# Kernel optimization log

Measured on AMD Instinct MI355X. Metric: run time of the kernel, lower is better.

## Reference

```python
import jax, jax.numpy as jnp
import numpy as np
from jax import lax

B, L, D, F = 32, 512, 256, 256
K = 3
EPS = 1e-5


def _layer_norm(h, g, b):
    mu = jnp.mean(h, axis=-1, keepdims=True)
    var = jnp.var(h, axis=-1, keepdims=True)
    return (h - mu) * lax.rsqrt(var + EPS) * g + b


def _conv1d(h, w, b):
    # h: [B, L, Cin], w: [K, Cin, Cout] -> [B, L, Cout], 'same' padding (pad=1, k=3)
    return lax.conv_general_dilated(h, w, window_strides=(1,), padding=[(1, 1)],
                                    dimension_numbers=('NWC', 'WIO', 'NWC')) + b


def _duration_predictor(x, c1w, c1b, ln1g, ln1b, c2w, c2b, ln2g, ln2b, lw, lb):
    h = jax.nn.relu(_layer_norm(_conv1d(x, c1w, c1b), ln1g, ln1b))
    h = jax.nn.relu(_layer_norm(_conv1d(h, c2w, c2b), ln2g, ln2b))
    d = jax.nn.relu(h @ lw + lb)  # [B, L, 1]
    return d[..., 0]              # [B, L] (squeeze, training mode)


def _expand_one(xb, dur, M):
    # xb: [L, D], dur: [L] int. Repeat row i dur[i] times, zero-pad to M frames.
    cs = jnp.cumsum(dur)                              # [L]
    t = jnp.arange(M)                                 # [M]
    idx = jnp.searchsorted(cs, t, side='right')       # phoneme id per frame
    valid = t < cs[-1]
    out = jnp.take(xb, jnp.clip(idx, 0, xb.shape[0] - 1), axis=0)
    return jnp.where(valid[:, None], out, jnp.zeros((), xb.dtype))


def setup_inputs() -> dict:
    key = jax.random.key(0)
    ks = jax.random.split(key, 8)
    s_c = 1.0 / np.sqrt(K * F)
    s_l = 1.0 / np.sqrt(F)
    return {
        'x': jax.random.normal(ks[0], (B, L, D), jnp.float32),
        'durations': jax.random.randint(ks[1], (B, L), 0, 7),
        'mel_max_length': 4096,
        'conv1_w': jax.random.normal(ks[2], (K, D, F), jnp.float32) * s_c,
        'conv1_b': jnp.zeros((F,), jnp.float32),
        'ln1_g': jnp.ones((F,), jnp.float32),
        'ln1_b': jnp.zeros((F,), jnp.float32),
        'conv2_w': jax.random.normal(ks[3], (K, F, F), jnp.float32) * s_c,
        'conv2_b': jnp.zeros((F,), jnp.float32),
        'ln2_g': jnp.ones((F,), jnp.float32),
        'ln2_b': jnp.zeros((F,), jnp.float32),
        'lin_w': jax.random.normal(ks[4], (F, 1), jnp.float32) * s_l,
        'lin_b': jnp.zeros((1,), jnp.float32),
    }


def reference(x, durations, mel_max_length, conv1_w, conv1_b, ln1_g, ln1_b,
              conv2_w, conv2_b, ln2_g, ln2_b, lin_w, lin_b):
    dur_pred = _duration_predictor(x, conv1_w, conv1_b, ln1_g, ln1_b,
                                   conv2_w, conv2_b, ln2_g, ln2_b, lin_w, lin_b)
    dur = durations.astype(jnp.int32)
    output = jax.vmap(lambda xb, db: _expand_one(xb, db, mel_max_length))(x, dur)
    return output, dur_pred
```

## Files before the change

### kernel.cpp

```cpp
#include <hip/hip_runtime.h>

typedef __attribute__((ext_vector_type(8))) short short8;
typedef __attribute__((ext_vector_type(4))) float f32x4;

#define BATCH 32
#define LSEQ  512
#define DIN   256
#define FDIM  256
#define KTOT  768
#define MT    32
#define BK    32
#define PADA  264

__device__ __forceinline__ short f2bf(float f) {
    union { float f; unsigned u; } v; v.f = f;
    unsigned r = v.u + 0x7FFFu + ((v.u >> 16) & 1u);
    return (short)(r >> 16);
}

__global__ __launch_bounds__(512)
void prep_kernel(const int* __restrict__ dur, int* __restrict__ cs,
                 const float* __restrict__ w1, const float* __restrict__ w2,
                 short* __restrict__ wt1, short* __restrict__ wt2) {
    __shared__ int s[LSEQ];
    const int t = threadIdx.x, b = blockIdx.x;
    if (b < BATCH) {
        s[t] = dur[b * LSEQ + t];
        __syncthreads();
        for (int off = 1; off < LSEQ; off <<= 1) {
            int v = (t >= off) ? s[t - off] : 0;
            __syncthreads();
            s[t] += v;
            __syncthreads();
        }
        cs[b * LSEQ + t] = s[t];
    } else {
        const int id = (b - BATCH) * 512 + t;
        const int n = id & 255, k = id >> 8;
        const int dst = (((k >> 5) * FDIM) + n) * BK + (k & 31);
        wt1[dst] = f2bf(w1[id]);
        wt2[dst] = f2bf(w2[id]);
    }
}

template<bool AF32, bool FUSE>
__global__ __launch_bounds__(256)
void conv_ln(const void* __restrict__ Asrc, const short* __restrict__ Bt,
             const float* __restrict__ cb, const float* __restrict__ g,
             const float* __restrict__ bta, const float* __restrict__ lw,
             const float* __restrict__ lb, short* __restrict__ Hout,
             float* __restrict__ Dout)
{
    __shared__ short As[34][PADA];
    __shared__ float redS[MT][4];
    __shared__ float redQ[MT][4];
    __shared__ float redD[MT][4];
    __shared__ float muS[MT];
    __shared__ float rsS[MT];

    const int tid  = threadIdx.x;
    const int wave = tid >> 6;
    const int lane = tid & 63;
    const int ml   = lane & 15;
    const int q    = lane >> 4;
    const int row0 = blockIdx.x * MT;
    const int bb   = row0 >> 9;
    const int r0   = row0 & (LSEQ - 1);

    for (int idx = tid; idx < 34 * 32; idx += 256) {
        const int r = idx >> 5, part = idx & 31;
        const int l2 = r0 + r - 1;
        short8 v = {0, 0, 0, 0, 0, 0, 0, 0};
        if (l2 >= 0 && l2 < LSEQ) {
            const size_t off = ((size_t)(bb * LSEQ + l2)) * DIN + part * 8;
            if (AF32) {
                const float4* s4 = (const float4*)((const float*)Asrc + off);
                float4 u0 = s4[0], u1 = s4[1];
                v[0] = f2bf(u0.x); v[1] = f2bf(u0.y); v[2] = f2bf(u0.z); v[3] = f2bf(u0.w);
                v[4] = f2bf(u1.x); v[5] = f2bf(u1.y); v[6] = f2bf(u1.z); v[7] = f2bf(u1.w);
            } else {
                v = *(const short8*)((const short*)Asrc + off);
            }
        }
        *(short8*)&As[r][part * 8] = v;
    }
    __syncthreads();

    f32x4 acc[2][4];
    #pragma unroll
    for (int mt = 0; mt < 2; mt++)
        #pragma unroll
        for (int nt = 0; nt < 4; nt++)
            #pragma unroll
            for (int r = 0; r < 4; r++)
                acc[mt][nt][r] = 0.f;

    const short* bptr = Bt + (size_t)(wave * 64 + ml) * BK + q * 8;
    #pragma unroll 1
    for (int tap = 0; tap < 3; tap++) {
        #pragma unroll
        for (int cc = 0; cc < 8; cc++) {
            short8 af0 = *(const short8*)&As[ml + tap][cc * 32 + q * 8];
            short8 af1 = *(const short8*)&As[16 + ml + tap][cc * 32 + q * 8];
            short8 b0 = *(const short8*)(bptr + 0 * 16 * BK);
            short8 b1 = *(const short8*)(bptr + 1 * 16 * BK);
            short8 b2 = *(const short8*)(bptr + 2 * 16 * BK);
            short8 b3 = *(const short8*)(bptr + 3 * 16 * BK);
            bptr += FDIM * BK;
            acc[0][0] = __builtin_amdgcn_mfma_f32_16x16x32_bf16(af0, b0, acc[0][0], 0, 0, 0);
            acc[0][1] = __builtin_amdgcn_mfma_f32_16x16x32_bf16(af0, b1, acc[0][1], 0, 0, 0);
            acc[0][2] = __builtin_amdgcn_mfma_f32_16x16x32_bf16(af0, b2, acc[0][2], 0, 0, 0);
            acc[0][3] = __builtin_amdgcn_mfma_f32_16x16x32_bf16(af0, b3, acc[0][3], 0, 0, 0);
            acc[1][0] = __builtin_amdgcn_mfma_f32_16x16x32_bf16(af1, b0, acc[1][0], 0, 0, 0);
            acc[1][1] = __builtin_amdgcn_mfma_f32_16x16x32_bf16(af1, b1, acc[1][1], 0, 0, 0);
            acc[1][2] = __builtin_amdgcn_mfma_f32_16x16x32_bf16(af1, b2, acc[1][2], 0, 0, 0);
            acc[1][3] = __builtin_amdgcn_mfma_f32_16x16x32_bf16(af1, b3, acc[1][3], 0, 0, 0);
        }
    }

    float cbv[4], gv[4], bv[4], lwv[4];
    #pragma unroll
    for (int nt = 0; nt < 4; nt++) {
        const int col = wave * 64 + nt * 16 + ml;
        cbv[nt] = cb[col]; gv[nt] = g[col]; bv[nt] = bta[col];
        lwv[nt] = FUSE ? lw[col] : 0.f;
    }
    #pragma unroll
    for (int mt = 0; mt < 2; mt++)
        #pragma unroll
        for (int nt = 0; nt < 4; nt++)
            #pragma unroll
            for (int r = 0; r < 4; r++)
                acc[mt][nt][r] += cbv[nt];

    #pragma unroll
    for (int mt = 0; mt < 2; mt++)
        #pragma unroll
        for (int r = 0; r < 4; r++) {
            float ps = 0.f, pq = 0.f;
            #pragma unroll
            for (int nt = 0; nt < 4; nt++) { float v = acc[mt][nt][r]; ps += v; pq += v * v; }
            #pragma unroll
            for (int d = 1; d < 16; d <<= 1) { ps += __shfl_xor(ps, d); pq += __shfl_xor(pq, d); }
            if (ml == 0) { const int row = mt * 16 + q * 4 + r; redS[row][wave] = ps; redQ[row][wave] = pq; }
        }
    __syncthreads();
    if (tid < MT) {
        float S = 0.f, Q = 0.f;
        #pragma unroll
        for (int w = 0; w < 4; w++) { S += redS[tid][w]; Q += redQ[tid][w]; }
        const float mu  = S * (1.f / 256.f);
        const float var = Q * (1.f / 256.f) - mu * mu;
        muS[tid] = mu; rsS[tid] = rsqrtf(var + 1e-5f);
    }
    __syncthreads();

    if (!FUSE) {
        #pragma unroll
        for (int mt = 0; mt < 2; mt++)
            #pragma unroll
            for (int r = 0; r < 4; r++) {
                const int row = mt * 16 + q * 4 + r;
                const float mu = muS[row], rs = rsS[row];
                #pragma unroll
                for (int nt = 0; nt < 4; nt++) {
                    const int col = wave * 64 + nt * 16 + ml;
                    float v = (acc[mt][nt][r] - mu) * rs * gv[nt] + bv[nt];
                    v = fmaxf(v, 0.f);
                    Hout[(size_t)(row0 + row) * FDIM + col] = f2bf(v);
                }
            }
    } else {
        #pragma unroll
        for (int mt = 0; mt < 2; mt++)
            #pragma unroll
            for (int r = 0; r < 4; r++) {
                const int row = mt * 16 + q * 4 + r;
                const float mu = muS[row], rs = rsS[row];
                float pd = 0.f;
                #pragma unroll
                for (int nt = 0; nt < 4; nt++) {
                    float v = (acc[mt][nt][r] - mu) * rs * gv[nt] + bv[nt];
                    v = fmaxf(v, 0.f);
                    pd += v * lwv[nt];
                }
                #pragma unroll
                for (int d = 1; d < 16; d <<= 1) pd += __shfl_xor(pd, d);
                if (ml == 0) redD[row][wave] = pd;
            }
        __syncthreads();
        if (tid < MT) {
            float Dv = 0.f;
            #pragma unroll
            for (int w = 0; w < 4; w++) Dv += redD[tid][w];
            Dout[row0 + tid] = fmaxf(Dv + lb[0], 0.f);
        }
    }
}

__global__ __launch_bounds__(256)
void expand_kernel(const float4* __restrict__ x4, const int* __restrict__ cs,
                   float4* __restrict__ out4, int M) {
    const int fr   = blockIdx.x * 4 + (threadIdx.x >> 6);
    const int lane = threadIdx.x & 63;
    const int b = fr / M;
    const int t = fr - b * M;
    const int* csb = cs + b * LSEQ;
    const int total = csb[LSEQ - 1];
    const size_t obase = (size_t)fr * 64 + lane;
    if (t < total) {
        int lo = 0, hi = LSEQ;
        while (lo < hi) { const int mid = (lo + hi) >> 1; if (csb[mid] > t) hi = mid; else lo = mid + 1; }
        const int idx = lo < LSEQ ? lo : LSEQ - 1;
        out4[obase] = x4[((size_t)(b * LSEQ + idx)) * 64 + lane];
    } else {
        out4[obase] = make_float4(0.f, 0.f, 0.f, 0.f);
    }
}

extern "C" void kernel_launch(void* const* d_in, const int* in_sizes, int n_in,
                              void* d_out, int out_size, void* d_ws, size_t ws_size,
                              hipStream_t stream)
{
    const float* x   = (const float*)d_in[0];
    const int*   dur = (const int*)d_in[1];
    const float* c1w = (const float*)d_in[3];
    const float* c1b = (const float*)d_in[4];
    const float* g1  = (const float*)d_in[5];
    const float* b1  = (const float*)d_in[6];
    const float* c2w = (const float*)d_in[7];
    const float* c2b = (const float*)d_in[8];
    const float* g2  = (const float*)d_in[9];
    const float* b2  = (const float*)d_in[10];
    const float* lw  = (const float*)d_in[11];
    const float* lb  = (const float*)d_in[12];

    const int M = (out_size - BATCH * LSEQ) / (BATCH * DIN);
    float* out     = (float*)d_out;
    float* dur_out = out + (size_t)BATCH * M * DIN;

    char* ws   = (char*)d_ws;
    int*   cs  = (int*)ws;
    short* wt1 = (short*)(ws + (64 << 10));
    short* wt2 = (short*)(ws + (64 << 10) + (384 << 10));
    short* h1  = (short*)(ws + (64 << 10) + 2 * (384 << 10));

    hipLaunchKernelGGL(prep_kernel, dim3(BATCH + (KTOT * FDIM) / 512), dim3(512), 0, stream,
                       dur, cs, c1w, c2w, wt1, wt2);
    hipLaunchKernelGGL((conv_ln<true, false>), dim3((BATCH * LSEQ) / MT), dim3(256), 0, stream,
                       (const void*)x, wt1, c1b, g1, b1, (const float*)nullptr, (const float*)nullptr,
                       h1, (float*)nullptr);
    hipLaunchKernelGGL((conv_ln<false, true>), dim3((BATCH * LSEQ) / MT), dim3(256), 0, stream,
                       (const void*)h1, wt2, c2b, g2, b2, lw, lb,
                       (short*)nullptr, dur_out);
    hipLaunchKernelGGL(expand_kernel, dim3((BATCH * M) / 4), dim3(256), 0, stream,
                       (const float4*)x, cs, (float4*)d_out, M);
}
```

Baseline: 214.9 us.

## Precompute frame index map and split expand work into conv kernels

The prep kernel now scatters a per-frame source row index (or -1 for padding) instead of storing cumulative sums, so expansion becomes a direct gather with no binary search. The standalone expand kernel is removed, and its blocks are split between the two conv+layernorm kernels as extra leading blocks. The aim is to overlap memory-bound output writes with compute-bound conv work and drop one launch. In exchange, the prep kernel does serial per-phoneme writes and initialises M entries per batch, and the workspace grows.

```diff
diff --git a/kernel.cpp b/kernel.cpp
--- a/kernel.cpp
+++ b/kernel.cpp
@@ -19,7 +19,7 @@
 }
 
 __global__ __launch_bounds__(512)
-void prep_kernel(const int* __restrict__ dur, int* __restrict__ cs,
+void prep_kernel(const int* __restrict__ dur, int* __restrict__ fidx, int M,
                  const float* __restrict__ w1, const float* __restrict__ w2,
                  short* __restrict__ wt1, short* __restrict__ wt2) {
     __shared__ int s[LSEQ];
@@ -33,7 +33,12 @@
             s[t] += v;
             __syncthreads();
         }
-        cs[b * LSEQ + t] = s[t];
+        for (int f = t; f < M; f += 512) fidx[b * M + f] = -1;
+        __syncthreads();
+        int lo = (t == 0) ? 0 : s[t - 1];
+        int hi = s[t];
+        if (hi > M) hi = M;
+        for (int j = lo; j < hi; j++) fidx[b * M + j] = b * LSEQ + t;
     } else {
         const int id = (b - BATCH) * 512 + t;
         const int n = id & 255, k = id >> 8;
@@ -45,11 +50,13 @@
 
 template<bool AF32, bool FUSE>
 __global__ __launch_bounds__(256)
-void conv_ln(const void* __restrict__ Asrc, const short* __restrict__ Bt,
-             const float* __restrict__ cb, const float* __restrict__ g,
-             const float* __restrict__ bta, const float* __restrict__ lw,
-             const float* __restrict__ lb, short* __restrict__ Hout,
-             float* __restrict__ Dout)
+void conv_ln_expand(const void* __restrict__ Asrc, const short* __restrict__ Bt,
+                    const float* __restrict__ cb, const float* __restrict__ g,
+                    const float* __restrict__ bta, const float* __restrict__ lw,
+                    const float* __restrict__ lb, short* __restrict__ Hout,
+                    float* __restrict__ Dout,
+                    const float4* __restrict__ x4, const int* __restrict__ fidx,
+                    float4* __restrict__ out4, int M, int nexp, int ebase)
 {
     __shared__ short As[34][PADA];
     __shared__ float redS[MT][4];
@@ -59,11 +66,22 @@
     __shared__ float rsS[MT];
 
     const int tid  = threadIdx.x;
+    const int lane = tid & 63;
+
+    if (blockIdx.x < (unsigned)nexp) {
+        const int fr = (ebase + blockIdx.x) * 4 + (tid >> 6);
+        const int idx = fidx[fr];
+        const size_t obase = (size_t)fr * 64 + lane;
+        if (idx >= 0) out4[obase] = x4[(size_t)idx * 64 + lane];
+        else          out4[obase] = make_float4(0.f, 0.f, 0.f, 0.f);
+        return;
+    }
+
+    const int cblk = blockIdx.x - nexp;
     const int wave = tid >> 6;
-    const int lane = tid & 63;
     const int ml   = lane & 15;
     const int q    = lane >> 4;
-    const int row0 = blockIdx.x * MT;
+    const int row0 = cblk * MT;
     const int bb   = row0 >> 9;
     const int r0   = row0 & (LSEQ - 1);
 
@@ -198,26 +216,6 @@
     }
 }
 
-__global__ __launch_bounds__(256)
-void expand_kernel(const float4* __restrict__ x4, const int* __restrict__ cs,
-                   float4* __restrict__ out4, int M) {
-    const int fr   = blockIdx.x * 4 + (threadIdx.x >> 6);
-    const int lane = threadIdx.x & 63;
-    const int b = fr / M;
-    const int t = fr - b * M;
-    const int* csb = cs + b * LSEQ;
-    const int total = csb[LSEQ - 1];
-    const size_t obase = (size_t)fr * 64 + lane;
-    if (t < total) {
-        int lo = 0, hi = LSEQ;
-        while (lo < hi) { const int mid = (lo + hi) >> 1; if (csb[mid] > t) hi = mid; else lo = mid + 1; }
-        const int idx = lo < LSEQ ? lo : LSEQ - 1;
-        out4[obase] = x4[((size_t)(b * LSEQ + idx)) * 64 + lane];
-    } else {
-        out4[obase] = make_float4(0.f, 0.f, 0.f, 0.f);
-    }
-}
-
 extern "C" void kernel_launch(void* const* d_in, const int* in_sizes, int n_in,
                               void* d_out, int out_size, void* d_ws, size_t ws_size,
                               hipStream_t stream)
@@ -240,19 +238,24 @@
     float* dur_out = out + (size_t)BATCH * M * DIN;
 
     char* ws   = (char*)d_ws;
-    int*   cs  = (int*)ws;
-    short* wt1 = (short*)(ws + (64 << 10));
-    short* wt2 = (short*)(ws + (64 << 10) + (384 << 10));
-    short* h1  = (short*)(ws + (64 << 10) + 2 * (384 << 10));
+    int*  fidx = (int*)ws;
+    short* wt1 = (short*)(ws + (512 << 10));
+    short* wt2 = (short*)(ws + (512 << 10) + (384 << 10));
+    short* h1  = (short*)(ws + (512 << 10) + 2 * (384 << 10));
+
+    const int NCONV = (BATCH * LSEQ) / MT;
+    const int NEXP  = (BATCH * M) / 4;
+    const int E1    = NEXP / 2;
+    const int E2    = NEXP - E1;
 
     hipLaunchKernelGGL(prep_kernel, dim3(BATCH + (KTOT * FDIM) / 512), dim3(512), 0, stream,
-                       dur, cs, c1w, c2w, wt1, wt2);
-    hipLaunchKernelGGL((conv_ln<true, false>), dim3((BATCH * LSEQ) / MT), dim3(256), 0, stream,
+                       dur, fidx, M, c1w, c2w, wt1, wt2);
+    hipLaunchKernelGGL((conv_ln_expand<true, false>), dim3(E1 + NCONV), dim3(256), 0, stream,
                        (const void*)x, wt1, c1b, g1, b1, (const float*)nullptr, (const float*)nullptr,
-                       h1, (float*)nullptr);
-    hipLaunchKernelGGL((conv_ln<false, true>), dim3((BATCH * LSEQ) / MT), dim3(256), 0, stream,
+                       h1, (float*)nullptr,
+                       (const float4*)x, fidx, (float4*)d_out, M, E1, 0);
+    hipLaunchKernelGGL((conv_ln_expand<false, true>), dim3(E2 + NCONV), dim3(256), 0, stream,
                        (const void*)h1, wt2, c2b, g2, b2, lw, lb,
-                       (short*)nullptr, dur_out);
-    hipLaunchKernelGGL(expand_kernel, dim3((BATCH * M) / 4), dim3(256), 0, stream,
-                       (const float4*)x, cs, (float4*)d_out, M);
-}
+                       (short*)nullptr, dur_out,
+                       (const float4*)x, fidx, (float4*)d_out, M, E2, E1);
+}
```

Result: slower. 241.8 us (+12.5%).
